# Performance work log

Hardware: AMD Instinct MI355X
Metric: run time of the kernel (lower is better)

## Reference

```python
import jax, jax.numpy as jnp
import numpy as np

QMIN, QMAX = -128.0, 127.0  # int8 range


def setup_inputs() -> dict:
    key = jax.random.key(0)
    k1, k2, k3, k4 = jax.random.split(key, 4)
    B, S, K, O = 8, 2048, 4096, 4096
    x = jax.random.normal(k1, (B, S, K), dtype=jnp.float32)
    weight = jax.random.normal(k2, (O, K), dtype=jnp.float32)
    bias = jax.random.normal(k3, (O,), dtype=jnp.float32)
    # per-tensor activation qparams (static, from calibration observer)
    act_scale = jnp.ones((1,), dtype=jnp.float32) * 0.05
    act_zp = jnp.zeros((1,), dtype=jnp.int32)
    # per-output-row weight qparams (block_size = (1, in_features))
    weight_scale = jax.random.uniform(k4, (O, 1), dtype=jnp.float32,
                                      minval=0.005, maxval=0.02)
    weight_zp = jnp.zeros((O, 1), dtype=jnp.int32)
    return {"x": x, "weight": weight, "bias": bias,
            "act_scale": act_scale, "weight_scale": weight_scale,
            "act_zp": act_zp, "weight_zp": weight_zp}


def _quant_dequant(v, scale, zp):
    # affine quantize to int8 grid, then dequantize (simulated int8 math)
    q = jnp.clip(jnp.round(v / scale) + zp.astype(v.dtype), QMIN, QMAX)
    return (q - zp.astype(v.dtype)) * scale


def reference(x, weight, bias, act_scale, weight_scale, act_zp, weight_zp):
    # static per-tensor activation quantization
    dqx = _quant_dequant(x, act_scale, act_zp)          # [B, S, K]
    # per-row weight quantization
    dqw = _quant_dequant(weight, weight_scale, weight_zp)  # [O, K]
    # F.linear: x @ W^T + b
    return jnp.einsum('bsk,ok->bso', dqx, dqw) + bias
```

## Files before the change

### kernel.cpp

```cpp
#include <hip/hip_runtime.h>
#include <cstdint>
#include <cstddef>

typedef __attribute__((ext_vector_type(4))) int   i32x4;
typedef __attribute__((ext_vector_type(4))) float f32x4;

#define M_DIM 16384
#define N_DIM 4096
#define K_DIM 4096
#define NT    (K_DIM / 128)

__global__ __launch_bounds__(256) void quant_x_kernel(
    const float* __restrict__ x,
    const float* __restrict__ act_scale,
    const int*   __restrict__ act_zp,
    signed char* __restrict__ xq)
{
    int idx = blockIdx.x * 256 + threadIdx.x;
    float s   = act_scale[0];
    float zpf = (float)act_zp[0];
    const f32x4* xp = (const f32x4*)(x + (size_t)idx * 16);
    union { signed char c[16]; i32x4 v; } u;
#pragma unroll
    for (int j = 0; j < 4; ++j) {
        f32x4 v = xp[j];
#pragma unroll
        for (int e = 0; e < 4; ++e) {
            float q = rintf(v[e] / s) + zpf;
            q = fminf(fmaxf(q, -128.f), 127.f);
            u.c[j * 4 + e] = (signed char)(int)(q - zpf);
        }
    }
    *(i32x4*)(xq + (size_t)idx * 16) = u.v;
}

__global__ __launch_bounds__(256) void quant_w_kernel(
    const float* __restrict__ w,
    const float* __restrict__ wscale,
    const int*   __restrict__ wzp,
    signed char* __restrict__ wq)
{
    int idx = blockIdx.x * 256 + threadIdx.x;
    int row = idx >> 8;
    float s   = wscale[row];
    float zpf = (float)wzp[row];
    const f32x4* wp = (const f32x4*)(w + (size_t)idx * 16);
    union { signed char c[16]; i32x4 v; } u;
#pragma unroll
    for (int j = 0; j < 4; ++j) {
        f32x4 v = wp[j];
#pragma unroll
        for (int e = 0; e < 4; ++e) {
            float q = rintf(v[e] / s) + zpf;
            q = fminf(fmaxf(q, -128.f), 127.f);
            u.c[j * 4 + e] = (signed char)(int)(q - zpf);
        }
    }
    *(i32x4*)(wq + (size_t)idx * 16) = u.v;
}

__global__ __launch_bounds__(512, 2) void gemm_i8_256(
    const signed char* __restrict__ Aq,
    const signed char* __restrict__ Bq,
    const float* __restrict__ bias,
    const float* __restrict__ act_scale,
    const float* __restrict__ wscale,
    float* __restrict__ out)
{
    __shared__ signed char lds[131072];

    const int nbn = N_DIM / 256;
    const int nwg = (M_DIM / 256) * nbn;
    int bid = blockIdx.x;
    int wg  = (bid & 7) * (nwg >> 3) + (bid >> 3);
    int bm  = wg / nbn;
    int bn  = wg % nbn;

    int tid  = threadIdx.x;
    int wave = tid >> 6;
    int lane = tid & 63;
    int wm_i = wave >> 2;
    int wn_i = wave & 3;

    const signed char* Ag = Aq + (size_t)bm * 256 * K_DIM;
    const signed char* Bg = Bq + (size_t)bn * 256 * K_DIM;

    int srow = tid >> 3;
    int scol = ((tid & 7) * 16) ^ ((srow & 7) << 4);
    int soff0 = srow * K_DIM + scol;
    int soff1 = (srow + 64) * K_DIM + scol;

    int lk = (lane >> 4) * 16;
    int xm = (lane & 7) << 4;
    int arow = wm_i * 128 + (lane & 15);
    int brow = wn_i * 64 + (lane & 15);
    int ab0 = (arow * 128 + lk) ^ xm;
    int ab1 = (arow * 128 + lk + 64) ^ xm;
    int bb0 = (32768 + brow * 128 + lk) ^ xm;
    int bb1 = (32768 + brow * 128 + lk + 64) ^ xm;

#define STAGE(tile, pos) do {                                                        \
    const signed char* _src = (((pos) < 2)                                           \
        ? (Bg + (size_t)((pos) * 128) * K_DIM)                                       \
        : (Ag + (size_t)(((pos) - 2) * 128) * K_DIM)) + (size_t)(tile) * 128;        \
    int _ldso = ((tile) & 1) * 65536                                                 \
              + (((pos) < 2) ? (32768 + (pos) * 16384) : (((pos) - 2) * 16384))      \
              + wave * 1024;                                                         \
    __builtin_amdgcn_global_load_lds(                                                \
        (const __attribute__((address_space(1))) void*)(_src + soff0),               \
        (__attribute__((address_space(3))) void*)(lds + _ldso), 16, 0, 0);           \
    __builtin_amdgcn_global_load_lds(                                                \
        (const __attribute__((address_space(1))) void*)(_src + soff1),               \
        (__attribute__((address_space(3))) void*)(lds + _ldso + 8192), 16, 0, 0);    \
} while (0)

    i32x4 acc[8][4] = {};
    i32x4 a0[4][2], a1[4][2], b0[2][2], b1[2][2];

    STAGE(0, 0); STAGE(0, 1); STAGE(0, 2); STAGE(0, 3);
    STAGE(1, 0); STAGE(1, 1);
    asm volatile("s_waitcnt vmcnt(4)" ::: "memory");
    __builtin_amdgcn_s_barrier();

    for (int t = 0; t < NT; ++t) {
        const signed char* buf = lds + (t & 1) * 65536;

#pragma unroll
        for (int mf = 0; mf < 4; ++mf) {
            a0[mf][0] = *(const i32x4*)(buf + ab0 + mf * 2048);
            a0[mf][1] = *(const i32x4*)(buf + ab1 + mf * 2048);
        }
#pragma unroll
        for (int nf = 0; nf < 2; ++nf) {
            b0[nf][0] = *(const i32x4*)(buf + bb0 + nf * 2048);
            b0[nf][1] = *(const i32x4*)(buf + bb1 + nf * 2048);
        }
        if (t + 1 < NT) STAGE(t + 1, 2);
        __builtin_amdgcn_s_barrier();
        __builtin_amdgcn_s_setprio(1);
#pragma unroll
        for (int mf = 0; mf < 4; ++mf)
#pragma unroll
            for (int nf = 0; nf < 2; ++nf)
#pragma unroll
                for (int kk = 0; kk < 2; ++kk)
                    acc[mf][nf] = __builtin_amdgcn_mfma_i32_16x16x64_i8(
                        a0[mf][kk], b0[nf][kk], acc[mf][nf], 0, 0, 0);
        __builtin_amdgcn_s_setprio(0);
        __builtin_amdgcn_s_barrier();

#pragma unroll
        for (int nf = 0; nf < 2; ++nf) {
            b1[nf][0] = *(const i32x4*)(buf + bb0 + (2 + nf) * 2048);
            b1[nf][1] = *(const i32x4*)(buf + bb1 + (2 + nf) * 2048);
        }
        if (t + 1 < NT) STAGE(t + 1, 3);
        __builtin_amdgcn_s_barrier();
        __builtin_amdgcn_s_setprio(1);
#pragma unroll
        for (int mf = 0; mf < 4; ++mf)
#pragma unroll
            for (int nf = 0; nf < 2; ++nf)
#pragma unroll
                for (int kk = 0; kk < 2; ++kk)
                    acc[mf][2 + nf] = __builtin_amdgcn_mfma_i32_16x16x64_i8(
                        a0[mf][kk], b1[nf][kk], acc[mf][2 + nf], 0, 0, 0);
        __builtin_amdgcn_s_setprio(0);
        __builtin_amdgcn_s_barrier();

#pragma unroll
        for (int mf = 0; mf < 4; ++mf) {
            a1[mf][0] = *(const i32x4*)(buf + ab0 + (4 + mf) * 2048);
            a1[mf][1] = *(const i32x4*)(buf + ab1 + (4 + mf) * 2048);
        }
        if (t + 2 < NT) STAGE(t + 2, 0);
        __builtin_amdgcn_s_barrier();
        __builtin_amdgcn_s_setprio(1);
#pragma unroll
        for (int mf = 0; mf < 4; ++mf)
#pragma unroll
            for (int nf = 0; nf < 2; ++nf)
#pragma unroll
                for (int kk = 0; kk < 2; ++kk)
                    acc[4 + mf][2 + nf] = __builtin_amdgcn_mfma_i32_16x16x64_i8(
                        a1[mf][kk], b1[nf][kk], acc[4 + mf][2 + nf], 0, 0, 0);
        __builtin_amdgcn_s_setprio(0);
        __builtin_amdgcn_s_barrier();

        if (t + 2 < NT) STAGE(t + 2, 1);
        __builtin_amdgcn_s_barrier();
        __builtin_amdgcn_s_setprio(1);
#pragma unroll
        for (int mf = 0; mf < 4; ++mf)
#pragma unroll
            for (int nf = 0; nf < 2; ++nf)
#pragma unroll
                for (int kk = 0; kk < 2; ++kk)
                    acc[4 + mf][nf] = __builtin_amdgcn_mfma_i32_16x16x64_i8(
                        a1[mf][kk], b0[nf][kk], acc[4 + mf][nf], 0, 0, 0);
        __builtin_amdgcn_s_setprio(0);
        if (t < NT - 2) {
            asm volatile("s_waitcnt vmcnt(4)" ::: "memory");
            __builtin_amdgcn_s_barrier();
        } else if (t == NT - 2) {
            asm volatile("s_waitcnt vmcnt(0)" ::: "memory");
            __builtin_amdgcn_s_barrier();
        }
    }
#undef STAGE

    float sa = act_scale[0];
    int colb = lane & 15;
    int rsub = (lane >> 4) * 4;
#pragma unroll
    for (int nf = 0; nf < 4; ++nf) {
        int o = bn * 256 + wn_i * 64 + nf * 16 + colb;
        float sw = sa * wscale[o];
        float bv = bias[o];
#pragma unroll
        for (int mf = 0; mf < 8; ++mf) {
            int grow = bm * 256 + wm_i * 128 + mf * 16 + rsub;
#pragma unroll
            for (int r = 0; r < 4; ++r)
                out[(size_t)(grow + r) * N_DIM + o] = (float)acc[mf][nf][r] * sw + bv;
        }
    }
}

__global__ void fallback_kernel(
    const float* __restrict__ x, const float* __restrict__ w,
    const float* __restrict__ bias,
    const float* __restrict__ act_scale, const float* __restrict__ wscale,
    const int* __restrict__ act_zp, const int* __restrict__ wzp,
    float* __restrict__ out)
{
    size_t idx = (size_t)blockIdx.x * blockDim.x + threadIdx.x;
    if (idx >= (size_t)M_DIM * N_DIM) return;
    int m = (int)(idx >> 12);
    int o = (int)(idx & 4095);
    float sx = act_scale[0], zx = (float)act_zp[0];
    float sw = wscale[o],    zw = (float)wzp[o];
    float acc = 0.f;
    for (int k = 0; k < K_DIM; ++k) {
        float qx = fminf(fmaxf(rintf(x[(size_t)m * K_DIM + k] / sx) + zx, -128.f), 127.f) - zx;
        float qw = fminf(fmaxf(rintf(w[(size_t)o * K_DIM + k] / sw) + zw, -128.f), 127.f) - zw;
        acc += (qx * sx) * (qw * sw);
    }
    out[idx] = acc + bias[o];
}

extern "C" void kernel_launch(void* const* d_in, const int* in_sizes, int n_in,
                              void* d_out, int out_size, void* d_ws, size_t ws_size,
                              hipStream_t stream)
{
    const float* x    = (const float*)d_in[0];
    const float* w    = (const float*)d_in[1];
    const float* bias = (const float*)d_in[2];
    const float* asc  = (const float*)d_in[3];
    const float* wsc  = (const float*)d_in[4];
    const int*   azp  = (const int*)d_in[5];
    const int*   wzp  = (const int*)d_in[6];
    float* out = (float*)d_out;

    size_t xq_bytes = (size_t)M_DIM * K_DIM;
    size_t wq_bytes = (size_t)N_DIM * K_DIM;

    if (ws_size < xq_bytes + wq_bytes) {
        int total = M_DIM * N_DIM;
        fallback_kernel<<<(total + 255) / 256, 256, 0, stream>>>(
            x, w, bias, asc, wsc, azp, wzp, out);
        return;
    }

    signed char* xq = (signed char*)d_ws;
    signed char* wq = (signed char*)d_ws + xq_bytes;

    quant_x_kernel<<<(M_DIM * (K_DIM / 16)) / 256, 256, 0, stream>>>(x, asc, azp, xq);
    quant_w_kernel<<<(N_DIM * (K_DIM / 16)) / 256, 256, 0, stream>>>(w, wsc, wzp, wq);
    gemm_i8_256<<<(M_DIM / 256) * (N_DIM / 256), 512, 0, stream>>>(
        xq, wq, bias, asc, wsc, out);
}
```

Measured before the change: 363.7 us.

## Prefetch next tile's LDS fragments during current MFMA phase and cut barriers

Restructures the int8 GEMM main loop so that LDS fragment reads for the next phase (B1, A1, and the next tile's A0/B0) are issued before the current MFMA block rather than behind a separate barrier. This halves the barriers per k-tile, from eight to four. The loop is unrolled by two with ping-pong A0/B0 register sets so the next tile's fragments load while the last quadrant computes. The global-to-LDS stage schedule and vmcnt waits are adjusted to match. It raises register pressure and makes correctness depend on the reordered barrier and waitcnt placement.

```diff
diff --git a/kernel.cpp b/kernel.cpp
--- a/kernel.cpp
+++ b/kernel.cpp
@@ -115,98 +115,91 @@
 } while (0)
 
     i32x4 acc[8][4] = {};
-    i32x4 a0[4][2], a1[4][2], b0[2][2], b1[2][2];
+    i32x4 a0E[4][2], b0E[2][2], a0O[4][2], b0O[2][2];
+    i32x4 a1[4][2], b1[2][2];
+
+#define MFMA_Q(AF, BF, mo, no) do {                                                  \
+    _Pragma("unroll")                                                                \
+    for (int mf = 0; mf < 4; ++mf)                                                   \
+        _Pragma("unroll")                                                            \
+        for (int nf = 0; nf < 2; ++nf)                                               \
+            _Pragma("unroll")                                                        \
+            for (int kk = 0; kk < 2; ++kk)                                           \
+                acc[(mo) + mf][(no) + nf] = __builtin_amdgcn_mfma_i32_16x16x64_i8(   \
+                    AF[mf][kk], BF[nf][kk], acc[(mo) + mf][(no) + nf], 0, 0, 0);     \
+} while (0)
+
+#define READ_B1(buf) do {                                                            \
+    _Pragma("unroll")                                                                \
+    for (int nf = 0; nf < 2; ++nf) {                                                 \
+        b1[nf][0] = *(const i32x4*)((buf) + bb0 + (2 + nf) * 2048);                  \
+        b1[nf][1] = *(const i32x4*)((buf) + bb1 + (2 + nf) * 2048);                  \
+    }                                                                                \
+} while (0)
+
+#define READ_A1(buf) do {                                                            \
+    _Pragma("unroll")                                                                \
+    for (int mf = 0; mf < 4; ++mf) {                                                 \
+        a1[mf][0] = *(const i32x4*)((buf) + ab0 + (4 + mf) * 2048);                  \
+        a1[mf][1] = *(const i32x4*)((buf) + ab1 + (4 + mf) * 2048);                  \
+    }                                                                                \
+} while (0)
+
+#define READ_A0B0(buf, A0, B0) do {                                                  \
+    _Pragma("unroll")                                                                \
+    for (int mf = 0; mf < 4; ++mf) {                                                 \
+        A0[mf][0] = *(const i32x4*)((buf) + ab0 + mf * 2048);                        \
+        A0[mf][1] = *(const i32x4*)((buf) + ab1 + mf * 2048);                        \
+    }                                                                                \
+    _Pragma("unroll")                                                                \
+    for (int nf = 0; nf < 2; ++nf) {                                                 \
+        B0[nf][0] = *(const i32x4*)((buf) + bb0 + nf * 2048);                        \
+        B0[nf][1] = *(const i32x4*)((buf) + bb1 + nf * 2048);                        \
+    }                                                                                \
+} while (0)
+
+#define TILE_BODY(t, bufc, bufn, A0c, B0c, A0n, B0n) do {                            \
+                                                                             \
+    READ_B1(bufc);                                                                   \
+    if ((t) + 1 < NT) STAGE((t) + 1, 2);                                             \
+    __builtin_amdgcn_s_setprio(1);  MFMA_Q(A0c, B0c, 0, 0);                          \
+    __builtin_amdgcn_s_setprio(0);  __builtin_amdgcn_s_barrier();                    \
+                                                                             \
+    READ_A1(bufc);                                                                   \
+    if ((t) + 1 < NT) STAGE((t) + 1, 3);                                             \
+    __builtin_amdgcn_s_setprio(1);  MFMA_Q(A0c, b1, 0, 2);                           \
+    __builtin_amdgcn_s_setprio(0);  __builtin_amdgcn_s_barrier();                    \
+                                                                             \
+    if ((t) + 2 < NT) STAGE((t) + 2, 0);                                             \
+    __builtin_amdgcn_s_setprio(1);  MFMA_Q(a1, b1, 4, 2);                            \
+    __builtin_amdgcn_s_setprio(0);                                                   \
+    if ((t) < NT - 2)       asm volatile("s_waitcnt vmcnt(2)" ::: "memory");         \
+    else if ((t) == NT - 2) asm volatile("s_waitcnt vmcnt(0)" ::: "memory");         \
+    __builtin_amdgcn_s_barrier();                                                    \
+                                                                             \
+    if ((t) + 1 < NT) READ_A0B0(bufn, A0n, B0n);                                     \
+    if ((t) + 2 < NT) STAGE((t) + 2, 1);                                             \
+    __builtin_amdgcn_s_setprio(1);  MFMA_Q(a1, B0c, 4, 0);                           \
+    __builtin_amdgcn_s_setprio(0);  __builtin_amdgcn_s_barrier();                    \
+} while (0)
 
     STAGE(0, 0); STAGE(0, 1); STAGE(0, 2); STAGE(0, 3);
-    STAGE(1, 0); STAGE(1, 1);
-    asm volatile("s_waitcnt vmcnt(4)" ::: "memory");
+    STAGE(1, 0);
+    asm volatile("s_waitcnt vmcnt(2)" ::: "memory");
     __builtin_amdgcn_s_barrier();
-
-    for (int t = 0; t < NT; ++t) {
-        const signed char* buf = lds + (t & 1) * 65536;
-
-#pragma unroll
-        for (int mf = 0; mf < 4; ++mf) {
-            a0[mf][0] = *(const i32x4*)(buf + ab0 + mf * 2048);
-            a0[mf][1] = *(const i32x4*)(buf + ab1 + mf * 2048);
-        }
-#pragma unroll
-        for (int nf = 0; nf < 2; ++nf) {
-            b0[nf][0] = *(const i32x4*)(buf + bb0 + nf * 2048);
-            b0[nf][1] = *(const i32x4*)(buf + bb1 + nf * 2048);
-        }
-        if (t + 1 < NT) STAGE(t + 1, 2);
-        __builtin_amdgcn_s_barrier();
-        __builtin_amdgcn_s_setprio(1);
-#pragma unroll
-        for (int mf = 0; mf < 4; ++mf)
-#pragma unroll
-            for (int nf = 0; nf < 2; ++nf)
-#pragma unroll
-                for (int kk = 0; kk < 2; ++kk)
-                    acc[mf][nf] = __builtin_amdgcn_mfma_i32_16x16x64_i8(
-                        a0[mf][kk], b0[nf][kk], acc[mf][nf], 0, 0, 0);
-        __builtin_amdgcn_s_setprio(0);
-        __builtin_amdgcn_s_barrier();
-
-#pragma unroll
-        for (int nf = 0; nf < 2; ++nf) {
-            b1[nf][0] = *(const i32x4*)(buf + bb0 + (2 + nf) * 2048);
-            b1[nf][1] = *(const i32x4*)(buf + bb1 + (2 + nf) * 2048);
-        }
-        if (t + 1 < NT) STAGE(t + 1, 3);
-        __builtin_amdgcn_s_barrier();
-        __builtin_amdgcn_s_setprio(1);
-#pragma unroll
-        for (int mf = 0; mf < 4; ++mf)
-#pragma unroll
-            for (int nf = 0; nf < 2; ++nf)
-#pragma unroll
-                for (int kk = 0; kk < 2; ++kk)
-                    acc[mf][2 + nf] = __builtin_amdgcn_mfma_i32_16x16x64_i8(
-                        a0[mf][kk], b1[nf][kk], acc[mf][2 + nf], 0, 0, 0);
-        __builtin_amdgcn_s_setprio(0);
-        __builtin_amdgcn_s_barrier();
-
-#pragma unroll
-        for (int mf = 0; mf < 4; ++mf) {
-            a1[mf][0] = *(const i32x4*)(buf + ab0 + (4 + mf) * 2048);
-            a1[mf][1] = *(const i32x4*)(buf + ab1 + (4 + mf) * 2048);
-        }
-        if (t + 2 < NT) STAGE(t + 2, 0);
-        __builtin_amdgcn_s_barrier();
-        __builtin_amdgcn_s_setprio(1);
-#pragma unroll
-        for (int mf = 0; mf < 4; ++mf)
-#pragma unroll
-            for (int nf = 0; nf < 2; ++nf)
-#pragma unroll
-                for (int kk = 0; kk < 2; ++kk)
-                    acc[4 + mf][2 + nf] = __builtin_amdgcn_mfma_i32_16x16x64_i8(
-                        a1[mf][kk], b1[nf][kk], acc[4 + mf][2 + nf], 0, 0, 0);
-        __builtin_amdgcn_s_setprio(0);
-        __builtin_amdgcn_s_barrier();
-
-        if (t + 2 < NT) STAGE(t + 2, 1);
-        __builtin_amdgcn_s_barrier();
-        __builtin_amdgcn_s_setprio(1);
-#pragma unroll
-        for (int mf = 0; mf < 4; ++mf)
-#pragma unroll
-            for (int nf = 0; nf < 2; ++nf)
-#pragma unroll
-                for (int kk = 0; kk < 2; ++kk)
-                    acc[4 + mf][nf] = __builtin_amdgcn_mfma_i32_16x16x64_i8(
-                        a1[mf][kk], b0[nf][kk], acc[4 + mf][nf], 0, 0, 0);
-        __builtin_amdgcn_s_setprio(0);
-        if (t < NT - 2) {
-            asm volatile("s_waitcnt vmcnt(4)" ::: "memory");
-            __builtin_amdgcn_s_barrier();
-        } else if (t == NT - 2) {
-            asm volatile("s_waitcnt vmcnt(0)" ::: "memory");
-            __builtin_amdgcn_s_barrier();
-        }
-    }
+    READ_A0B0(lds, a0E, b0E);
+    STAGE(1, 1);
+    __builtin_amdgcn_s_barrier();
+
+    for (int tt = 0; tt < NT; tt += 2) {
+        TILE_BODY(tt,     lds,         lds + 65536, a0E, b0E, a0O, b0O);
+        TILE_BODY(tt + 1, lds + 65536, lds,         a0O, b0O, a0E, b0E);
+    }
+#undef TILE_BODY
+#undef READ_A0B0
+#undef READ_A1
+#undef READ_B1
+#undef MFMA_Q
 #undef STAGE
 
     float sa = act_scale[0];
```

Result: slower. 768.5 us (+111.3%).
